# Optimization experiments

Hardware: AMD Instinct MI355X
Metric: run time of the kernel (lower is better)

## Reference

```python
import jax, jax.numpy as jnp
import numpy as np

VOCAB, E, H, L, B, T = 32000, 64, 8, 25, 1000, 512


def setup_inputs() -> dict:
    key = jax.random.key(0)
    ks = jax.random.split(key, 6)
    return {
        "x": jax.random.randint(ks[0], (B, T), 0, VOCAB),
        "h_0": jnp.zeros((L, B, H), jnp.float32),
        "embedding": jax.random.normal(ks[1], (VOCAB, E), jnp.float32) * 0.02,
        "W_xh0": jax.random.normal(ks[2], (E, H), jnp.float32) / np.float32(np.sqrt(E)),
        "W_xh_rest": jax.random.normal(ks[3], (L - 1, H, H), jnp.float32) / np.float32(np.sqrt(H)),
        "W_hh": jax.random.normal(ks[4], (L, H, H), jnp.float32) / np.float32(np.sqrt(H)),
        "b_h": jnp.zeros((L, H), jnp.float32),
        "W_hy": jax.random.normal(ks[5], (H, 1), jnp.float32) / np.float32(np.sqrt(H)),
        "b_y": jnp.zeros((1,), jnp.float32),
    }


def reference(x, h_0, embedding, W_xh0, W_xh_rest, W_hh, b_h, W_hy, b_y):
    # x: [B, T] int ids; embedded: [B, T, E]
    emb = embedding[x]
    n_layers = h_0.shape[0]

    def step(h, e_t):  # h: [L, B, H], e_t: [B, E]
        inp = e_t
        hs = []
        for i in range(n_layers):  # fixed small layer count -> unrolled
            W = W_xh0 if i == 0 else W_xh_rest[i - 1]
            h_i = jnp.tanh(inp @ W + h[i] @ W_hh[i] + b_h[i])
            hs.append(h_i)
            inp = h_i
        return jnp.stack(hs, 0), None

    h_last, _ = jax.lax.scan(step, h_0, jnp.swapaxes(emb, 0, 1))  # scan over time
    logits = h_last[-1] @ W_hy + b_y  # [B, 1]
    return logits.squeeze(1), h_last
```

## Files before the change

kernel.cpp:

```cpp
#include <hip/hip_runtime.h>

#define VOCAB 32000
#define E 64
#define H 8
#define L 25
#define B 1000
#define T 512

#define CHUNK 8
#define NCHUNK (T / CHUNK)
#define NSTEP (NCHUNK + L - 1)
#define THREADS 256

#define LAYER_STRIDE 132
#define LDS_FLOATS (L * LAYER_STRIDE)

typedef float v2f __attribute__((ext_vector_type(2)));

__global__ __launch_bounds__(256) void proj_kernel(
    const float* __restrict__ emb, const float* __restrict__ w0,
    float* __restrict__ ptab)
{
    __shared__ float w0s[E * H];
    int tid = threadIdx.x;
    w0s[tid] = w0[tid];
    w0s[tid + 256] = w0[tid + 256];
    __syncthreads();

    int gid = blockIdx.x * 256 + tid;
    if (gid >= VOCAB * H) return;
    int j = gid & 7;
    int r = gid >> 3;
    const float4* e4 = (const float4*)(emb + r * E);
    float a0 = 0.f, a1 = 0.f, a2 = 0.f, a3 = 0.f;
#pragma unroll
    for (int k4 = 0; k4 < E / 4; ++k4) {
        float4 v = e4[k4];
        a0 += v.x * w0s[(4 * k4 + 0) * H + j];
        a1 += v.y * w0s[(4 * k4 + 1) * H + j];
        a2 += v.z * w0s[(4 * k4 + 2) * H + j];
        a3 += v.w * w0s[(4 * k4 + 3) * H + j];
    }
    ptab[gid] = (a0 + a1) + (a2 + a3);
}

__device__ __forceinline__ float fast_tanh(float x) {
    float e2 = __expf(2.0f * x);
    return 1.0f - 2.0f / (e2 + 1.0f);
}

__device__ __forceinline__ float fxor1(float x) {
    return __int_as_float(__builtin_amdgcn_mov_dpp(__float_as_int(x), 0xB1, 0xF, 0xF, true));
}
__device__ __forceinline__ float fxor2(float x) {
    return __int_as_float(__builtin_amdgcn_mov_dpp(__float_as_int(x), 0x4E, 0xF, 0xF, true));
}
__device__ __forceinline__ float fxor4(float x) {
    return __int_as_float(__builtin_amdgcn_ds_swizzle(__float_as_int(x), 0x101F));
}

__global__ __launch_bounds__(THREADS) void rnn_recur(
    const int*   __restrict__ x,
    const float* __restrict__ h0,
    const float* __restrict__ wrest,
    const float* __restrict__ whh_g,
    const float* __restrict__ bh,
    const float* __restrict__ why,
    const float* __restrict__ by,
    const float* __restrict__ ptab,
    float*       __restrict__ out)
{
    __shared__ __align__(16) float buf[LDS_FLOATS];

    const int tid = threadIdx.x;
    const int i = tid >> 3;
    const int j = tid & 7;
    const bool active = tid < L * H;
    const int b = blockIdx.x;

    v2f wh01 = {0.f, 0.f}, wh23 = {0.f, 0.f}, wh45 = {0.f, 0.f}, wh67 = {0.f, 0.f};
    v2f wx01 = {0.f, 0.f}, wx23 = {0.f, 0.f}, wx45 = {0.f, 0.f}, wx67 = {0.f, 0.f};
    v2f h01  = {0.f, 0.f}, h23  = {0.f, 0.f}, h45  = {0.f, 0.f}, h67  = {0.f, 0.f};
    float bias = 0.f, byv = 0.f;
    float wy0 = 0.f, wy1 = 0.f, wy2 = 0.f, wy3 = 0.f,
          wy4 = 0.f, wy5 = 0.f, wy6 = 0.f, wy7 = 0.f;

    float* mybuf = &buf[i * LAYER_STRIDE];
    const float* prevbuf = mybuf - LAYER_STRIDE;

    if (active) {
        const float* whL = whh_g + i * 64;
        wh01 = (v2f){whL[(j ^ 0) * 8 + j], whL[(j ^ 1) * 8 + j]};
        wh23 = (v2f){whL[(j ^ 2) * 8 + j], whL[(j ^ 3) * 8 + j]};
        wh45 = (v2f){whL[(j ^ 4) * 8 + j], whL[(j ^ 5) * 8 + j]};
        wh67 = (v2f){whL[(j ^ 6) * 8 + j], whL[(j ^ 7) * 8 + j]};
        if (i > 0) {
            const float* wxL = wrest + (i - 1) * 64;
            wx01 = (v2f){wxL[0 * 8 + j], wxL[1 * 8 + j]};
            wx23 = (v2f){wxL[2 * 8 + j], wxL[3 * 8 + j]};
            wx45 = (v2f){wxL[4 * 8 + j], wxL[5 * 8 + j]};
            wx67 = (v2f){wxL[6 * 8 + j], wxL[7 * 8 + j]};
        }
        bias = bh[i * 8 + j];
        const float* h0p = h0 + (i * B + b) * H;
        h01 = (v2f){h0p[j ^ 0], h0p[j ^ 1]};
        h23 = (v2f){h0p[j ^ 2], h0p[j ^ 3]};
        h45 = (v2f){h0p[j ^ 4], h0p[j ^ 5]};
        h67 = (v2f){h0p[j ^ 6], h0p[j ^ 7]};
        if (i == L - 1) {
            wy0 = why[j ^ 0]; wy1 = why[j ^ 1]; wy2 = why[j ^ 2]; wy3 = why[j ^ 3];
            wy4 = why[j ^ 4]; wy5 = why[j ^ 5]; wy6 = why[j ^ 6]; wy7 = why[j ^ 7];
            byv = by[0];
        }
    }

    const int xbase = b * T;
    float pv[CHUNK];
    if (active && i == 0) {
#pragma unroll
        for (int ct = 0; ct < CHUNK; ++ct)
            pv[ct] = ptab[x[xbase + ct] * H + j];
    }

    for (int s = 0; s < NSTEP; ++s) {
        const int c = s - i;
        if (active && (unsigned)c < (unsigned)NCHUNK) {
            const int p = c & 1;
            float* wptr = mybuf + p * (CHUNK * 8);
            const float* iptr = prevbuf + p * (CHUNK * 8);

            int tokn[CHUNK];
            const bool pf = (i == 0) && (c + 1 < NCHUNK);
            if (pf) {
#pragma unroll
                for (int ct = 0; ct < CHUNK; ++ct)
                    tokn[ct] = x[xbase + (c + 1) * CHUNK + ct];
            }

#pragma unroll
            for (int ct = 0; ct < CHUNK; ++ct) {
                v2f acc, acc2;
                if (i == 0) {
                    acc  = (v2f){pv[ct] + bias, 0.f};
                    acc2 = (v2f){0.f, 0.f};
                } else {
                    float4 ia = *(const float4*)(iptr + ct * 8);
                    float4 ib = *(const float4*)(iptr + ct * 8 + 4);
                    acc   = (v2f){bias, 0.f};
                    acc  += (v2f){ia.x, ia.y} * wx01;
                    acc2  = (v2f){ia.z, ia.w} * wx23;
                    acc  += (v2f){ib.x, ib.y} * wx45;
                    acc2 += (v2f){ib.z, ib.w} * wx67;
                }
                acc  += h01 * wh01;
                acc2 += h23 * wh23;
                acc  += h45 * wh45;
                acc2 += h67 * wh67;
                v2f at = acc + acc2;
                float hn = fast_tanh(at.x + at.y);

                if (i < L - 1) wptr[ct * 8 + j] = hn;

                float o1 = fxor1(hn);
                float p0 = fxor2(hn);
                float p1 = fxor2(o1);
                h01 = (v2f){hn, o1};
                h23 = (v2f){p0, p1};
                h45 = (v2f){fxor4(hn), fxor4(o1)};
                h67 = (v2f){fxor4(p0), fxor4(p1)};
            }

            if (pf) {
#pragma unroll
                for (int ct = 0; ct < CHUNK; ++ct)
                    pv[ct] = ptab[tokn[ct] * H + j];
            }

            if (c == NCHUNK - 1) {
                out[B + (i * B + b) * H + j] = h01.x;
                if (i == L - 1) {
                    float lg = byv;
                    lg += h01.x * wy0 + h01.y * wy1;
                    lg += h23.x * wy2 + h23.y * wy3;
                    lg += h45.x * wy4 + h45.y * wy5;
                    lg += h67.x * wy6 + h67.y * wy7;
                    if (j == 0) out[b] = lg;
                }
            }
        }
        __syncthreads();
    }
}

extern "C" void kernel_launch(void* const* d_in, const int* in_sizes, int n_in,
                              void* d_out, int out_size, void* d_ws, size_t ws_size,
                              hipStream_t stream) {
    const int*   x     = (const int*)d_in[0];
    const float* h0    = (const float*)d_in[1];
    const float* emb   = (const float*)d_in[2];
    const float* w0    = (const float*)d_in[3];
    const float* wrest = (const float*)d_in[4];
    const float* whh   = (const float*)d_in[5];
    const float* bh    = (const float*)d_in[6];
    const float* why   = (const float*)d_in[7];
    const float* by    = (const float*)d_in[8];
    float* out  = (float*)d_out;
    float* ptab = (float*)d_ws;

    hipLaunchKernelGGL(proj_kernel, dim3((VOCAB * H + 255) / 256), dim3(256),
                       0, stream, emb, w0, ptab);
    hipLaunchKernelGGL(rnn_recur, dim3(B), dim3(THREADS),
                       0, stream, x, h0, wrest, whh, bh, why, by, ptab, out);
}
```

Baseline: 271.9 us.

## Remap lanes so all hidden-state exchanges use DPP; batch LDS input loads

```diff
diff --git a/kernel.cpp b/kernel.cpp
--- a/kernel.cpp
+++ b/kernel.cpp
@@ -27,36 +27,42 @@
     w0s[tid + 256] = w0[tid + 256];
     __syncthreads();
 
-    int gid = blockIdx.x * 256 + tid;
-    if (gid >= VOCAB * H) return;
-    int j = gid & 7;
-    int r = gid >> 3;
+    int r = blockIdx.x * 256 + tid;
+    if (r >= VOCAB) return;
     const float4* e4 = (const float4*)(emb + r * E);
-    float a0 = 0.f, a1 = 0.f, a2 = 0.f, a3 = 0.f;
+    const v2f* w2 = (const v2f*)w0s;
+    v2f a0 = {0.f, 0.f}, a1 = {0.f, 0.f}, a2 = {0.f, 0.f}, a3 = {0.f, 0.f};
 #pragma unroll
     for (int k4 = 0; k4 < E / 4; ++k4) {
         float4 v = e4[k4];
-        a0 += v.x * w0s[(4 * k4 + 0) * H + j];
-        a1 += v.y * w0s[(4 * k4 + 1) * H + j];
-        a2 += v.z * w0s[(4 * k4 + 2) * H + j];
-        a3 += v.w * w0s[(4 * k4 + 3) * H + j];
-    }
-    ptab[gid] = (a0 + a1) + (a2 + a3);
+        int kb = k4 * 16;
+        a0 += (v2f){v.x, v.x} * w2[kb + 0];  a1 += (v2f){v.x, v.x} * w2[kb + 1];
+        a2 += (v2f){v.x, v.x} * w2[kb + 2];  a3 += (v2f){v.x, v.x} * w2[kb + 3];
+        a0 += (v2f){v.y, v.y} * w2[kb + 4];  a1 += (v2f){v.y, v.y} * w2[kb + 5];
+        a2 += (v2f){v.y, v.y} * w2[kb + 6];  a3 += (v2f){v.y, v.y} * w2[kb + 7];
+        a0 += (v2f){v.z, v.z} * w2[kb + 8];  a1 += (v2f){v.z, v.z} * w2[kb + 9];
+        a2 += (v2f){v.z, v.z} * w2[kb + 10]; a3 += (v2f){v.z, v.z} * w2[kb + 11];
+        a0 += (v2f){v.w, v.w} * w2[kb + 12]; a1 += (v2f){v.w, v.w} * w2[kb + 13];
+        a2 += (v2f){v.w, v.w} * w2[kb + 14]; a3 += (v2f){v.w, v.w} * w2[kb + 15];
+    }
+    float4* o4 = (float4*)(ptab + r * 8);
+    o4[0] = (float4){a0.x, a0.y, a1.x, a1.y};
+    o4[1] = (float4){a2.x, a2.y, a3.x, a3.y};
 }
 
 __device__ __forceinline__ float fast_tanh(float x) {
-    float e2 = __expf(2.0f * x);
+    float e2 = exp2f(x * 2.8853900817779268f);
     return 1.0f - 2.0f / (e2 + 1.0f);
 }
 
-__device__ __forceinline__ float fxor1(float x) {
+__device__ __forceinline__ float dpp_xor1(float x) {
     return __int_as_float(__builtin_amdgcn_mov_dpp(__float_as_int(x), 0xB1, 0xF, 0xF, true));
 }
-__device__ __forceinline__ float fxor2(float x) {
+__device__ __forceinline__ float dpp_xor2(float x) {
     return __int_as_float(__builtin_amdgcn_mov_dpp(__float_as_int(x), 0x4E, 0xF, 0xF, true));
 }
-__device__ __forceinline__ float fxor4(float x) {
-    return __int_as_float(__builtin_amdgcn_ds_swizzle(__float_as_int(x), 0x101F));
+__device__ __forceinline__ float dpp_xor8(float x) {
+    return __int_as_float(__builtin_amdgcn_mov_dpp(__float_as_int(x), 0x128, 0xF, 0xF, true));
 }
 
 __global__ __launch_bounds__(THREADS) void rnn_recur(
@@ -73,9 +79,12 @@
     __shared__ __align__(16) float buf[LDS_FLOATS];
 
     const int tid = threadIdx.x;
-    const int i = tid >> 3;
-    const int j = tid & 7;
-    const bool active = tid < L * H;
+    const int row = tid >> 4;
+    const int lp  = tid & 15;
+    const int j   = (lp & 3) | ((lp >> 3) << 2);
+    const int g   = row * 2 + ((lp >> 2) & 1);
+    const bool active = g < L;
+    const int gc  = active ? g : 0;
     const int b = blockIdx.x;
 
     v2f wh01 = {0.f, 0.f}, wh23 = {0.f, 0.f}, wh45 = {0.f, 0.f}, wh67 = {0.f, 0.f};
@@ -85,29 +94,29 @@
     float wy0 = 0.f, wy1 = 0.f, wy2 = 0.f, wy3 = 0.f,
           wy4 = 0.f, wy5 = 0.f, wy6 = 0.f, wy7 = 0.f;
 
-    float* mybuf = &buf[i * LAYER_STRIDE];
-    const float* prevbuf = mybuf - LAYER_STRIDE;
+    float* mybuf = &buf[gc * LAYER_STRIDE];
+    const float* prevbuf = (gc > 0) ? (mybuf - LAYER_STRIDE) : mybuf;
 
     if (active) {
-        const float* whL = whh_g + i * 64;
+        const float* whL = whh_g + g * 64;
         wh01 = (v2f){whL[(j ^ 0) * 8 + j], whL[(j ^ 1) * 8 + j]};
         wh23 = (v2f){whL[(j ^ 2) * 8 + j], whL[(j ^ 3) * 8 + j]};
         wh45 = (v2f){whL[(j ^ 4) * 8 + j], whL[(j ^ 5) * 8 + j]};
         wh67 = (v2f){whL[(j ^ 6) * 8 + j], whL[(j ^ 7) * 8 + j]};
-        if (i > 0) {
-            const float* wxL = wrest + (i - 1) * 64;
+        if (g > 0) {
+            const float* wxL = wrest + (g - 1) * 64;
             wx01 = (v2f){wxL[0 * 8 + j], wxL[1 * 8 + j]};
             wx23 = (v2f){wxL[2 * 8 + j], wxL[3 * 8 + j]};
             wx45 = (v2f){wxL[4 * 8 + j], wxL[5 * 8 + j]};
             wx67 = (v2f){wxL[6 * 8 + j], wxL[7 * 8 + j]};
         }
-        bias = bh[i * 8 + j];
-        const float* h0p = h0 + (i * B + b) * H;
+        bias = bh[g * 8 + j];
+        const float* h0p = h0 + (g * B + b) * H;
         h01 = (v2f){h0p[j ^ 0], h0p[j ^ 1]};
         h23 = (v2f){h0p[j ^ 2], h0p[j ^ 3]};
         h45 = (v2f){h0p[j ^ 4], h0p[j ^ 5]};
         h67 = (v2f){h0p[j ^ 6], h0p[j ^ 7]};
-        if (i == L - 1) {
+        if (g == L - 1) {
             wy0 = why[j ^ 0]; wy1 = why[j ^ 1]; wy2 = why[j ^ 2]; wy3 = why[j ^ 3];
             wy4 = why[j ^ 4]; wy5 = why[j ^ 5]; wy6 = why[j ^ 6]; wy7 = why[j ^ 7];
             byv = by[0];
@@ -116,36 +125,44 @@
 
     const int xbase = b * T;
     float pv[CHUNK];
-    if (active && i == 0) {
+    if (active && g == 0) {
 #pragma unroll
         for (int ct = 0; ct < CHUNK; ++ct)
             pv[ct] = ptab[x[xbase + ct] * H + j];
     }
 
     for (int s = 0; s < NSTEP; ++s) {
-        const int c = s - i;
+        const int c = s - g;
         if (active && (unsigned)c < (unsigned)NCHUNK) {
             const int p = c & 1;
             float* wptr = mybuf + p * (CHUNK * 8);
-            const float* iptr = prevbuf + p * (CHUNK * 8);
 
             int tokn[CHUNK];
-            const bool pf = (i == 0) && (c + 1 < NCHUNK);
+            const bool pf = (g == 0) && (c + 1 < NCHUNK);
             if (pf) {
 #pragma unroll
                 for (int ct = 0; ct < CHUNK; ++ct)
                     tokn[ct] = x[xbase + (c + 1) * CHUNK + ct];
             }
 
+            float4 IA[CHUNK], IB[CHUNK];
+            if (g > 0) {
+                const float4* ip4 = (const float4*)(prevbuf + p * (CHUNK * 8));
+#pragma unroll
+                for (int ct = 0; ct < CHUNK; ++ct) {
+                    IA[ct] = ip4[2 * ct];
+                    IB[ct] = ip4[2 * ct + 1];
+                }
+            }
+
 #pragma unroll
             for (int ct = 0; ct < CHUNK; ++ct) {
                 v2f acc, acc2;
-                if (i == 0) {
+                if (g == 0) {
                     acc  = (v2f){pv[ct] + bias, 0.f};
                     acc2 = (v2f){0.f, 0.f};
                 } else {
-                    float4 ia = *(const float4*)(iptr + ct * 8);
-                    float4 ib = *(const float4*)(iptr + ct * 8 + 4);
+                    float4 ia = IA[ct], ib = IB[ct];
                     acc   = (v2f){bias, 0.f};
                     acc  += (v2f){ia.x, ia.y} * wx01;
                     acc2  = (v2f){ia.z, ia.w} * wx23;
@@ -159,15 +176,15 @@
                 v2f at = acc + acc2;
                 float hn = fast_tanh(at.x + at.y);
 
-                if (i < L - 1) wptr[ct * 8 + j] = hn;
-
-                float o1 = fxor1(hn);
-                float p0 = fxor2(hn);
-                float p1 = fxor2(o1);
+                if (g < L - 1) wptr[ct * 8 + j] = hn;
+
+                float o1 = dpp_xor1(hn);
+                float q0 = dpp_xor2(hn);
+                float q1 = dpp_xor2(o1);
                 h01 = (v2f){hn, o1};
-                h23 = (v2f){p0, p1};
-                h45 = (v2f){fxor4(hn), fxor4(o1)};
-                h67 = (v2f){fxor4(p0), fxor4(p1)};
+                h23 = (v2f){q0, q1};
+                h45 = (v2f){dpp_xor8(hn), dpp_xor8(o1)};
+                h67 = (v2f){dpp_xor8(q0), dpp_xor8(q1)};
             }
 
             if (pf) {
@@ -177,8 +194,8 @@
             }
 
             if (c == NCHUNK - 1) {
-                out[B + (i * B + b) * H + j] = h01.x;
-                if (i == L - 1) {
+                out[B + (g * B + b) * H + j] = h01.x;
+                if (g == L - 1) {
                     float lg = byv;
                     lg += h01.x * wy0 + h01.y * wy1;
                     lg += h23.x * wy2 + h23.y * wy3;
@@ -207,7 +224,7 @@
     float* out  = (float*)d_out;
     float* ptab = (float*)d_ws;
 
-    hipLaunchKernelGGL(proj_kernel, dim3((VOCAB * H + 255) / 256), dim3(256),
+    hipLaunchKernelGGL(proj_kernel, dim3((VOCAB + 255) / 256), dim3(256),
                        0, stream, emb, w0, ptab);
     hipLaunchKernelGGL(rnn_recur, dim3(B), dim3(THREADS),
                        0, stream, x, h0, wrest, whh, bh, why, by, ptab, out);
```

Result: slower. 320.8 us (+18.0%).
